# Performance work log

Hardware: AMD Instinct MI355X
Metric: run time of the kernel (lower is better)

The kernel has to match this reference:

```python
import jax, jax.numpy as jnp
import numpy as np

WH, WW = 7, 7           # window height/width
N = WH * WW             # tokens per window = 49
C = 768                 # num_channels
H = 24                  # num_heads
D = C // H              # head_dim = 32
B = 1024                # total windows (batch * windows-per-image)
NW = 64                 # windows per image (shift_mask leading dim)
EPS = 1e-5


def _relative_position_index():
    # Mirrors the torch buffer construction in __init__.
    coords = np.stack(np.meshgrid(np.arange(WH), np.arange(WW), indexing='ij'))  # [2,WH,WW]
    cf = coords.reshape(2, -1)                          # [2,N]
    rel = cf[:, :, None] - cf[:, None, :]               # [2,N,N]
    rel = rel.transpose(1, 2, 0).copy()                 # [N,N,2]
    rel[:, :, 0] += WH - 1
    rel[:, :, 1] += WW - 1
    rel[:, :, 0] *= 2 * WW - 1
    return jnp.asarray(rel.sum(-1), dtype=jnp.int32)    # [N,N]


def setup_inputs() -> dict:
    key = jax.random.key(0)
    ks = jax.random.split(key, 6)
    x = jax.random.normal(ks[0], (B, N, C), dtype=jnp.float32)
    shift_mask = jax.random.normal(ks[1], (NW, N, N), dtype=jnp.float32)
    w_qkv = jax.random.normal(ks[2], (3 * C, C), dtype=jnp.float32) * 0.02
    b_qkv = jnp.zeros((3 * C,), dtype=jnp.float32)
    w_proj = jax.random.normal(ks[3], (C, C), dtype=jnp.float32) * 0.02
    b_proj = jnp.zeros((C,), dtype=jnp.float32)
    rel_bias_table = jax.random.normal(ks[4], ((2 * WH - 1) * (2 * WW - 1), H), dtype=jnp.float32) * 0.02
    ln_g = jnp.ones((C,), dtype=jnp.float32)
    ln_b = jnp.zeros((C,), dtype=jnp.float32)
    rel_pos_index = _relative_position_index()
    return {
        'x': x, 'shift_mask': shift_mask,
        'w_qkv': w_qkv, 'b_qkv': b_qkv,
        'w_proj': w_proj, 'b_proj': b_proj,
        'rel_bias_table': rel_bias_table,
        'ln_g': ln_g, 'ln_b': ln_b,
        'rel_pos_index': rel_pos_index,
    }


def reference(x, shift_mask, w_qkv, b_qkv, w_proj, b_proj, rel_bias_table, ln_g, ln_b, rel_pos_index):
    B_, N_, C_ = x.shape
    # QKV projection: [B,N,3C] -> [3,B,H,N,D]
    qkv = (x @ w_qkv.T + b_qkv).reshape(B_, N_, 3, H, D).transpose(2, 0, 3, 1, 4)
    q, k, v = qkv[0], qkv[1], qkv[2]
    # Relative position bias gather: [N,N,H] -> [1,H,N,N]
    bias = rel_bias_table[rel_pos_index.reshape(-1)].reshape(N_, N_, H).transpose(2, 0, 1)[None]
    # Shift mask broadcast over batch repeats and heads: [B,1,N,N]
    mask = jnp.tile(shift_mask, (B_ // shift_mask.shape[0], 1, 1))[:, None]
    attn_bias = bias + mask  # [B,H,N,N]
    scale = 1.0 / np.sqrt(D).astype(np.float32)
    scores = jnp.einsum('bhnd,bhmd->bhnm', q, k) * scale + attn_bias
    attn = jax.nn.softmax(scores, axis=-1)
    out = jnp.einsum('bhnm,bhmd->bhnd', attn, v)       # [B,H,N,D]
    out = out.transpose(0, 2, 1, 3).reshape(B_, N_, C_)
    out = out @ w_proj.T + b_proj                      # dropout p=0 -> identity
    y = out + x
    mu = jnp.mean(y, axis=-1, keepdims=True)
    var = jnp.mean(jnp.square(y - mu), axis=-1, keepdims=True)
    return (y - mu) * jax.lax.rsqrt(var + EPS) * ln_g + ln_b
```

## Files before the change

kernel.cpp:

```cpp
#include <hip/hip_runtime.h>
#include <hip/hip_bf16.h>

#define SEQ 49
#define CH 768
#define NH 24
#define HD 32
#define NB 1024
#define NWIN 64
#define MTOT (NB*SEQ)

typedef __hip_bfloat16 bf16;
typedef __attribute__((ext_vector_type(8))) short short8;
typedef __attribute__((ext_vector_type(4))) short short4v;
typedef __attribute__((ext_vector_type(4))) float f32x4;

#define MD  ((size_t)MTOT * HD)
#define NHMD ((size_t)NH * MD)

__device__ __forceinline__ void gload16(const void* g, void* l) {
  __builtin_amdgcn_global_load_lds((__attribute__((address_space(1))) void*)g,
                                   (__attribute__((address_space(3))) void*)l,
                                   16, 0, 0);
}

__device__ __forceinline__ float bf2f(short s) {
  return __uint_as_float(((unsigned int)(unsigned short)s) << 16);
}

__global__ void cvt_bf16(const float* __restrict__ in, bf16* __restrict__ o, int n4) {
  int i = blockIdx.x * blockDim.x + threadIdx.x;
  if (i >= n4) return;
  float4 v = ((const float4*)in)[i];
  union { bf16 b[4]; short4 s; } u;
  u.b[0] = __float2bfloat16(v.x);
  u.b[1] = __float2bfloat16(v.y);
  u.b[2] = __float2bfloat16(v.z);
  u.b[3] = __float2bfloat16(v.w);
  ((short4*)o)[i] = u.s;
}

__global__ void build_comb(const float* __restrict__ table, const int* __restrict__ rpi,
                           const float* __restrict__ smask, float* __restrict__ comb) {
  int i = blockIdx.x * blockDim.x + threadIdx.x;
  int mn = i & 4095;
  int m = mn >> 6, n = mn & 63;
  int sh = i >> 12;
  int h = sh % NH;
  int s = sh / NH;
  float v = -1e30f;
  if (m < SEQ && n < SEQ)
    v = table[rpi[m * SEQ + n] * NH + h] + smask[s * SEQ * SEQ + m * SEQ + n];
  comb[i] = v;
}


__global__ __launch_bounds__(256) void qkv_gemm(
    const bf16* __restrict__ A, const bf16* __restrict__ Bw,
    const float* __restrict__ bias, bf16* __restrict__ C)
{
  __shared__ __align__(16) bf16 As[2 * 128 * 64];
  __shared__ __align__(16) bf16 Bs[2 * 128 * 64];
  const int tid = threadIdx.x;
  const int w = tid >> 6, l = tid & 63;
  const int lr = l & 15, lg = l >> 4;
  const int wm = w >> 1, wn = w & 1;

  const int flat = blockIdx.x;
  const int wg = (flat & 7) * 882 + (flat >> 3);
  const int bm = wg / 18, bn = wg - 18 * (wg / 18);

  const bf16* gA[4];
  const bf16* gB[4];
  int ldst[4];
#pragma unroll
  for (int j = 0; j < 4; j++) {
    int c = j * 256 + tid;
    int row = c >> 3, cpos = c & 7;
    int srcch = cpos ^ (row & 7);
    gA[j] = A + ((size_t)(bm * 128 + row)) * CH + srcch * 8;
    gB[j] = Bw + ((size_t)(bn * 128 + row)) * CH + srcch * 8;
    ldst[j] = c * 8;
  }

  f32x4 acc[4][4];
  f32x4 zero4 = {0.f, 0.f, 0.f, 0.f};
#pragma unroll
  for (int i = 0; i < 4; i++)
#pragma unroll
    for (int j = 0; j < 4; j++) acc[i][j] = zero4;

  int offA[4][2], offB[4][2];
#pragma unroll
  for (int mi = 0; mi < 4; mi++) {
#pragma unroll
    for (int ks = 0; ks < 2; ks++) {
      int rowa = 64 * wm + 16 * mi + lr;
      offA[mi][ks] = rowa * 64 + ((lg + 4 * ks) ^ (rowa & 7)) * 8;
      int rowb = 64 * wn + 16 * mi + lr;
      offB[mi][ks] = rowb * 64 + ((lg + 4 * ks) ^ (rowb & 7)) * 8;
    }
  }

#pragma unroll
  for (int j = 0; j < 4; j++) gload16(gA[j], As + ldst[j]);
#pragma unroll
  for (int j = 0; j < 4; j++) gload16(gB[j], Bs + ldst[j]);
#pragma unroll
  for (int j = 0; j < 4; j++) gload16(gA[j] + 64, As + 8192 + ldst[j]);
#pragma unroll
  for (int j = 0; j < 4; j++) gload16(gB[j] + 64, Bs + 8192 + ldst[j]);

  for (int t = 0; t < 12; ++t) {
    if (t < 11) asm volatile("s_waitcnt vmcnt(8)" ::: "memory");
    else        asm volatile("s_waitcnt vmcnt(0)" ::: "memory");
    __builtin_amdgcn_sched_barrier(0);
    __builtin_amdgcn_s_barrier();
    const int base = (t & 1) * 8192;
    const bf16* cA = As + base;
    const bf16* cB = Bs + base;
    short8 af[4][2], bfv[4][2];
#pragma unroll
    for (int mi = 0; mi < 4; mi++)
#pragma unroll
      for (int ks = 0; ks < 2; ks++) {
        af[mi][ks] = *(const short8*)(cA + offA[mi][ks]);
        bfv[mi][ks] = *(const short8*)(cB + offB[mi][ks]);
      }
    asm volatile("s_waitcnt lgkmcnt(0)" ::: "memory");
    __builtin_amdgcn_sched_barrier(0);
    __builtin_amdgcn_s_barrier();
    if (t < 10) {
      const int kk = (t + 2) * 64;
#pragma unroll
      for (int j = 0; j < 4; j++) gload16(gA[j] + kk, As + base + ldst[j]);
#pragma unroll
      for (int j = 0; j < 4; j++) gload16(gB[j] + kk, Bs + base + ldst[j]);
    }
    __builtin_amdgcn_s_setprio(1);
#pragma unroll
    for (int ks = 0; ks < 2; ks++)
#pragma unroll
      for (int mi = 0; mi < 4; mi++)
#pragma unroll
        for (int nj = 0; nj < 4; nj++)
          acc[mi][nj] = __builtin_amdgcn_mfma_f32_16x16x32_bf16(af[mi][ks], bfv[nj][ks], acc[mi][nj], 0, 0, 0);
    __builtin_amdgcn_s_setprio(0);
  }

  const float scale = 0.17677669529663687f;
  const int colbase = bn * 128 + 64 * wn;
  const int rowbase = bm * 128 + 64 * wm;
#pragma unroll
  for (int nj = 0; nj < 4; nj++) {
    const int cb16 = colbase + 16 * nj;
    const int sec = cb16 / 768;
    const int rem = cb16 - sec * 768;
    const int h = rem >> 5;
    const int dbase = rem & 31;
    float bv = bias[cb16 + lr];
    if (sec == 2) {
      const size_t vbase = 2 * NHMD + ((size_t)h * HD + dbase + lr) * MTOT;
#pragma unroll
      for (int mi = 0; mi < 4; mi++) {
        size_t row = rowbase + 16 * mi + 4 * lg;
        union { bf16 b[4]; short4 s; } u;
#pragma unroll
        for (int r = 0; r < 4; r++) u.b[r] = __float2bfloat16(acc[mi][nj][r] + bv);
        *(short4*)(C + vbase + row) = u.s;
      }
    } else {
      const float mul = (sec == 0) ? scale : 1.0f;
      const size_t base = (size_t)sec * NHMD + (size_t)h * MD + dbase + lr;
#pragma unroll
      for (int mi = 0; mi < 4; mi++) {
#pragma unroll
        for (int r = 0; r < 4; r++) {
          size_t row = rowbase + 16 * mi + 4 * lg + r;
          C[base + row * HD] = __float2bfloat16((acc[mi][nj][r] + bv) * mul);
        }
      }
    }
  }
}

__global__ __launch_bounds__(256) void attn_kernel(
    const bf16* __restrict__ qkvT, const float* __restrict__ comb,
    bf16* __restrict__ aout)
{
  __shared__ __align__(16) bf16 P[4][64 * 72];
  const int tid = threadIdx.x;
  const int w = tid >> 6, l = tid & 63;
  const int lr = l & 15, lg = l >> 4;
  const int b = blockIdx.x;
  const int h = blockIdx.y * 4 + w;
  const size_t rowb = (size_t)b * SEQ;
  f32x4 zero4 = {0.f, 0.f, 0.f, 0.f};

  const bf16* qb = qkvT + (size_t)h * MD + rowb * HD;
  const bf16* kb = qkvT + NHMD + (size_t)h * MD + rowb * HD;
  const bf16* vT = qkvT + 2 * NHMD + (size_t)h * HD * MTOT;

  short8 qf[4], kf[4];
#pragma unroll
  for (int mt = 0; mt < 4; mt++)
    qf[mt] = *(const short8*)(qb + (16 * mt + lr) * HD + 8 * lg);
#pragma unroll
  for (int nt = 0; nt < 4; nt++)
    kf[nt] = *(const short8*)(kb + (16 * nt + lr) * HD + 8 * lg);

  f32x4 s[4][4];
#pragma unroll
  for (int mt = 0; mt < 4; mt++)
#pragma unroll
    for (int nt = 0; nt < 4; nt++)
      s[mt][nt] = __builtin_amdgcn_mfma_f32_16x16x32_bf16(qf[mt], kf[nt], zero4, 0, 0, 0);

  short8 pb[2][2];
#pragma unroll
  for (int kt = 0; kt < 2; kt++)
#pragma unroll
    for (int dt = 0; dt < 2; dt++)
      pb[kt][dt] = *(const short8*)(vT + ((size_t)(16 * dt + lr)) * MTOT + rowb + 32 * kt + 8 * lg);

  const float* cb = comb + (((size_t)(b & (NWIN - 1)) * NH + h) << 12);
#pragma unroll
  for (int mt = 0; mt < 4; mt++)
#pragma unroll
    for (int nt = 0; nt < 4; nt++)
#pragma unroll
      for (int r = 0; r < 4; r++)
        s[mt][nt][r] += cb[((16 * mt + 4 * lg + r) << 6) + 16 * nt + lr];

  float mx[4][4];
#pragma unroll
  for (int mt = 0; mt < 4; mt++)
#pragma unroll
    for (int r = 0; r < 4; r++) {
      float m0 = fmaxf(fmaxf(s[mt][0][r], s[mt][1][r]), fmaxf(s[mt][2][r], s[mt][3][r]));
      m0 = fmaxf(m0, __shfl_xor(m0, 1, 64));
      m0 = fmaxf(m0, __shfl_xor(m0, 2, 64));
      m0 = fmaxf(m0, __shfl_xor(m0, 4, 64));
      m0 = fmaxf(m0, __shfl_xor(m0, 8, 64));
      mx[mt][r] = m0;
    }
  float inv[4][4];
#pragma unroll
  for (int mt = 0; mt < 4; mt++)
#pragma unroll
    for (int r = 0; r < 4; r++) {
      float t = 0.f;
#pragma unroll
      for (int nt = 0; nt < 4; nt++) {
        float e = __expf(s[mt][nt][r] - mx[mt][r]);
        s[mt][nt][r] = e;
        t += e;
      }
      t += __shfl_xor(t, 1, 64);
      t += __shfl_xor(t, 2, 64);
      t += __shfl_xor(t, 4, 64);
      t += __shfl_xor(t, 8, 64);
      inv[mt][r] = 1.0f / t;
    }

#pragma unroll
  for (int mt = 0; mt < 4; mt++)
#pragma unroll
    for (int nt = 0; nt < 4; nt++)
#pragma unroll
      for (int r = 0; r < 4; r++)
        P[w][(16 * mt + 4 * lg + r) * 72 + 16 * nt + lr] =
            __float2bfloat16(s[mt][nt][r]);

  f32x4 o[4][2];
#pragma unroll
  for (int mt = 0; mt < 4; mt++) { o[mt][0] = zero4; o[mt][1] = zero4; }
#pragma unroll
  for (int kt = 0; kt < 2; kt++) {
    short8 pa[4];
#pragma unroll
    for (int mt = 0; mt < 4; mt++)
      pa[mt] = *(const short8*)(&P[w][(16 * mt + lr) * 72 + 32 * kt + 8 * lg]);
#pragma unroll
    for (int mt = 0; mt < 4; mt++)
#pragma unroll
      for (int dt = 0; dt < 2; dt++)
        o[mt][dt] = __builtin_amdgcn_mfma_f32_16x16x32_bf16(pa[mt], pb[kt][dt], o[mt][dt], 0, 0, 0);
  }

#pragma unroll
  for (int mt = 0; mt < 4; mt++)
#pragma unroll
    for (int dt = 0; dt < 2; dt++)
#pragma unroll
      for (int r = 0; r < 4; r++) {
        int m = 16 * mt + 4 * lg + r;
        if (m < SEQ)
          aout[(rowb + m) * CH + h * HD + 16 * dt + lr] =
              __float2bfloat16(o[mt][dt][r] * inv[mt][r]);
      }
}

__global__ __launch_bounds__(256) void proj_gemm(
    const bf16* __restrict__ A, const bf16* __restrict__ Bw,
    const float* __restrict__ bias, const float* __restrict__ x,
    bf16* __restrict__ Y)
{
  __shared__ __align__(16) bf16 As[2 * 128 * 64];
  __shared__ __align__(16) bf16 Bs[2 * 128 * 64];
  const int tid = threadIdx.x;
  const int w = tid >> 6, l = tid & 63;
  const int lr = l & 15, lg = l >> 4;
  const int wm = w >> 1, wn = w & 1;

  const int flat = blockIdx.x;
  const int wg = (flat & 7) * 294 + (flat >> 3);
  const int bm = wg / 6, bn = wg - 6 * (wg / 6);

  const bf16* gA[4];
  const bf16* gB[4];
  int ldst[4];
#pragma unroll
  for (int j = 0; j < 4; j++) {
    int c = j * 256 + tid;
    int row = c >> 3, cpos = c & 7;
    int srcch = cpos ^ (row & 7);
    gA[j] = A + ((size_t)(bm * 128 + row)) * CH + srcch * 8;
    gB[j] = Bw + ((size_t)(bn * 128 + row)) * CH + srcch * 8;
    ldst[j] = c * 8;
  }

  f32x4 acc[4][4];
  f32x4 zero4 = {0.f, 0.f, 0.f, 0.f};
#pragma unroll
  for (int i = 0; i < 4; i++)
#pragma unroll
    for (int j = 0; j < 4; j++) acc[i][j] = zero4;

  int offA[4][2], offB[4][2];
#pragma unroll
  for (int mi = 0; mi < 4; mi++) {
#pragma unroll
    for (int ks = 0; ks < 2; ks++) {
      int rowa = 64 * wm + 16 * mi + lr;
      offA[mi][ks] = rowa * 64 + ((lg + 4 * ks) ^ (rowa & 7)) * 8;
      int rowb = 64 * wn + 16 * mi + lr;
      offB[mi][ks] = rowb * 64 + ((lg + 4 * ks) ^ (rowb & 7)) * 8;
    }
  }

#pragma unroll
  for (int j = 0; j < 4; j++) gload16(gA[j], As + ldst[j]);
#pragma unroll
  for (int j = 0; j < 4; j++) gload16(gB[j], Bs + ldst[j]);
#pragma unroll
  for (int j = 0; j < 4; j++) gload16(gA[j] + 64, As + 8192 + ldst[j]);
#pragma unroll
  for (int j = 0; j < 4; j++) gload16(gB[j] + 64, Bs + 8192 + ldst[j]);

  for (int t = 0; t < 12; ++t) {
    if (t < 11) asm volatile("s_waitcnt vmcnt(8)" ::: "memory");
    else        asm volatile("s_waitcnt vmcnt(0)" ::: "memory");
    __builtin_amdgcn_sched_barrier(0);
    __builtin_amdgcn_s_barrier();
    const int base = (t & 1) * 8192;
    const bf16* cA = As + base;
    const bf16* cB = Bs + base;
    short8 af[4][2], bfv[4][2];
#pragma unroll
    for (int mi = 0; mi < 4; mi++)
#pragma unroll
      for (int ks = 0; ks < 2; ks++) {
        af[mi][ks] = *(const short8*)(cA + offA[mi][ks]);
        bfv[mi][ks] = *(const short8*)(cB + offB[mi][ks]);
      }
    asm volatile("s_waitcnt lgkmcnt(0)" ::: "memory");
    __builtin_amdgcn_sched_barrier(0);
    __builtin_amdgcn_s_barrier();
    if (t < 10) {
      const int kk = (t + 2) * 64;
#pragma unroll
      for (int j = 0; j < 4; j++) gload16(gA[j] + kk, As + base + ldst[j]);
#pragma unroll
      for (int j = 0; j < 4; j++) gload16(gB[j] + kk, Bs + base + ldst[j]);
    }
    __builtin_amdgcn_s_setprio(1);
#pragma unroll
    for (int ks = 0; ks < 2; ks++)
#pragma unroll
      for (int mi = 0; mi < 4; mi++)
#pragma unroll
        for (int nj = 0; nj < 4; nj++)
          acc[mi][nj] = __builtin_amdgcn_mfma_f32_16x16x32_bf16(af[mi][ks], bfv[nj][ks], acc[mi][nj], 0, 0, 0);
    __builtin_amdgcn_s_setprio(0);
  }

  const int colbase = bn * 128 + 64 * wn;
  const int rowbase = bm * 128 + 64 * wm;
#pragma unroll
  for (int nj = 0; nj < 4; nj++) {
    int col = colbase + 16 * nj + lr;
    float bv = bias[col];
#pragma unroll
    for (int mi = 0; mi < 4; mi++) {
#pragma unroll
      for (int r = 0; r < 4; r++) {
        size_t row = rowbase + 16 * mi + 4 * lg + r;
        float v = acc[mi][nj][r] + bv + x[row * CH + col];
        Y[row * CH + col] = __float2bfloat16(v);
      }
    }
  }
}

__global__ __launch_bounds__(256) void ln_kernel(
    const bf16* __restrict__ Y, const float* __restrict__ g,
    const float* __restrict__ be, float* __restrict__ out)
{
  const int w = threadIdx.x >> 6, l = threadIdx.x & 63;
  const size_t r = (size_t)blockIdx.x * 4 + w;
  const bf16* yr = Y + r * CH;

  short8 a = *(const short8*)(yr + 8 * l);
  short4v b4 = *(const short4v*)(yr + 512 + 4 * l);
  float v[12];
#pragma unroll
  for (int j = 0; j < 8; j++) v[j] = bf2f(a[j]);
#pragma unroll
  for (int j = 0; j < 4; j++) v[8 + j] = bf2f(b4[j]);

  float s1 = 0.f, s2 = 0.f;
#pragma unroll
  for (int j = 0; j < 12; j++) { s1 += v[j]; s2 += v[j] * v[j]; }
#pragma unroll
  for (int m = 1; m <= 32; m <<= 1) {
    s1 += __shfl_xor(s1, m, 64);
    s2 += __shfl_xor(s2, m, 64);
  }
  float mu = s1 * (1.0f / 768.0f);
  float var = s2 * (1.0f / 768.0f) - mu * mu;
  float rs = rsqrtf(var + 1e-5f);

  float4 g0 = *(const float4*)(g + 8 * l);
  float4 g1 = *(const float4*)(g + 8 * l + 4);
  float4 g2 = *(const float4*)(g + 512 + 4 * l);
  float4 b0 = *(const float4*)(be + 8 * l);
  float4 b1 = *(const float4*)(be + 8 * l + 4);
  float4 b2 = *(const float4*)(be + 512 + 4 * l);

  float4 o0, o1, o2;
  o0.x = (v[0] - mu) * rs * g0.x + b0.x;
  o0.y = (v[1] - mu) * rs * g0.y + b0.y;
  o0.z = (v[2] - mu) * rs * g0.z + b0.z;
  o0.w = (v[3] - mu) * rs * g0.w + b0.w;
  o1.x = (v[4] - mu) * rs * g1.x + b1.x;
  o1.y = (v[5] - mu) * rs * g1.y + b1.y;
  o1.z = (v[6] - mu) * rs * g1.z + b1.z;
  o1.w = (v[7] - mu) * rs * g1.w + b1.w;
  o2.x = (v[8] - mu) * rs * g2.x + b2.x;
  o2.y = (v[9] - mu) * rs * g2.y + b2.y;
  o2.z = (v[10] - mu) * rs * g2.z + b2.z;
  o2.w = (v[11] - mu) * rs * g2.w + b2.w;

  float* orow = out + r * CH;
  *(float4*)(orow + 8 * l) = o0;
  *(float4*)(orow + 8 * l + 4) = o1;
  *(float4*)(orow + 512 + 4 * l) = o2;
}

extern "C" void kernel_launch(void* const* d_in, const int* in_sizes, int n_in,
                              void* d_out, int out_size, void* d_ws, size_t ws_size,
                              hipStream_t stream) {
  (void)in_sizes; (void)n_in; (void)out_size; (void)ws_size;
  const float* x     = (const float*)d_in[0];
  const float* smask = (const float*)d_in[1];
  const float* wqkv  = (const float*)d_in[2];
  const float* bqkv  = (const float*)d_in[3];
  const float* wproj = (const float*)d_in[4];
  const float* bproj = (const float*)d_in[5];
  const float* table = (const float*)d_in[6];
  const float* lng   = (const float*)d_in[7];
  const float* lnb   = (const float*)d_in[8];
  const int*   rpi   = (const int*)d_in[9];
  float* out = (float*)d_out;

  char* ws = (char*)d_ws;
  bf16*  xb   = (bf16*)(ws);
  bf16*  wqb  = (bf16*)(ws + 77070336);
  bf16*  wpb  = (bf16*)(ws + 80609280);
  float* comb = (float*)(ws + 81788928);
  bf16*  qkvT = (bf16*)(ws + 106954752);
  bf16*  aout = (bf16*)(ws);
  bf16*  yb   = (bf16*)(ws + 106954752);

  cvt_bf16<<<37632, 256, 0, stream>>>(x, xb, 9633792);
  cvt_bf16<<<1728, 256, 0, stream>>>(wqkv, wqb, 442368);
  cvt_bf16<<<576, 256, 0, stream>>>(wproj, wpb, 147456);
  build_comb<<<24576, 256, 0, stream>>>(table, rpi, smask, comb);
  qkv_gemm<<<7056, 256, 0, stream>>>(xb, wqb, bqkv, qkvT);
  attn_kernel<<<dim3(1024, 6), 256, 0, stream>>>(qkvT, comb, aout);
  proj_gemm<<<2352, 256, 0, stream>>>(aout, wpb, bproj, x, yb);
  ln_kernel<<<12544, 256, 0, stream>>>(yb, lng, lnb, out);
}
```

Baseline: 603.8 us.

## Enlarge QKV GEMM tile to 256x256 with 512 threads and 128KB LDS

The QKV GEMM moves from 128x128 tiles with 4 waves to 256x256 tiles with 8 waves, each computing 128x64. Shared memory becomes dynamic at 128KB for double-buffered A/B, and the XCD-aware block remap is updated for the new grid of 1764 blocks. The prefetch is restructured to issue the next K-slice at the top of each iteration, and fragments are loaded per k-step. The goal is higher arithmetic intensity and less global/LDS traffic per FLOP, at the cost of one block per CU, more accumulator registers and a shallower prefetch pipeline.

```diff
diff --git a/kernel.cpp b/kernel.cpp
--- a/kernel.cpp
+++ b/kernel.cpp
@@ -53,103 +53,105 @@
   comb[i] = v;
 }
 
-
-__global__ __launch_bounds__(256) void qkv_gemm(
+__global__ __launch_bounds__(512) void qkv_gemm(
     const bf16* __restrict__ A, const bf16* __restrict__ Bw,
     const float* __restrict__ bias, bf16* __restrict__ C)
 {
-  __shared__ __align__(16) bf16 As[2 * 128 * 64];
-  __shared__ __align__(16) bf16 Bs[2 * 128 * 64];
+  extern __shared__ __align__(16) bf16 lds[];
   const int tid = threadIdx.x;
   const int w = tid >> 6, l = tid & 63;
   const int lr = l & 15, lg = l >> 4;
-  const int wm = w >> 1, wn = w & 1;
+  const int wm = w >> 2, wn = w & 3;
 
   const int flat = blockIdx.x;
-  const int wg = (flat & 7) * 882 + (flat >> 3);
-  const int bm = wg / 18, bn = wg - 18 * (wg / 18);
+  const int xcd = flat & 7, lid = flat >> 3;
+  const int wgid = (xcd < 4 ? xcd * 221 : 884 + (xcd - 4) * 220) + lid;
+  const int bm = wgid / 9, bn = wgid - 9 * bm;
 
   const bf16* gA[4];
   const bf16* gB[4];
   int ldst[4];
 #pragma unroll
   for (int j = 0; j < 4; j++) {
-    int c = j * 256 + tid;
+    int c = j * 512 + tid;
     int row = c >> 3, cpos = c & 7;
     int srcch = cpos ^ (row & 7);
-    gA[j] = A + ((size_t)(bm * 128 + row)) * CH + srcch * 8;
-    gB[j] = Bw + ((size_t)(bn * 128 + row)) * CH + srcch * 8;
+    gA[j] = A + ((size_t)(bm * 256 + row)) * CH + srcch * 8;
+    gB[j] = Bw + ((size_t)(bn * 256 + row)) * CH + srcch * 8;
     ldst[j] = c * 8;
   }
 
-  f32x4 acc[4][4];
+  f32x4 acc[8][4];
   f32x4 zero4 = {0.f, 0.f, 0.f, 0.f};
 #pragma unroll
-  for (int i = 0; i < 4; i++)
+  for (int i = 0; i < 8; i++)
 #pragma unroll
     for (int j = 0; j < 4; j++) acc[i][j] = zero4;
 
-  int offA[4][2], offB[4][2];
-#pragma unroll
-  for (int mi = 0; mi < 4; mi++) {
+  int offA[8][2], offB[4][2];
+#pragma unroll
+  for (int mi = 0; mi < 8; mi++)
 #pragma unroll
     for (int ks = 0; ks < 2; ks++) {
-      int rowa = 64 * wm + 16 * mi + lr;
+      int rowa = wm * 128 + mi * 16 + lr;
       offA[mi][ks] = rowa * 64 + ((lg + 4 * ks) ^ (rowa & 7)) * 8;
-      int rowb = 64 * wn + 16 * mi + lr;
-      offB[mi][ks] = rowb * 64 + ((lg + 4 * ks) ^ (rowb & 7)) * 8;
-    }
-  }
-
-#pragma unroll
-  for (int j = 0; j < 4; j++) gload16(gA[j], As + ldst[j]);
-#pragma unroll
-  for (int j = 0; j < 4; j++) gload16(gB[j], Bs + ldst[j]);
-#pragma unroll
-  for (int j = 0; j < 4; j++) gload16(gA[j] + 64, As + 8192 + ldst[j]);
-#pragma unroll
-  for (int j = 0; j < 4; j++) gload16(gB[j] + 64, Bs + 8192 + ldst[j]);
+    }
+#pragma unroll
+  for (int nj = 0; nj < 4; nj++)
+#pragma unroll
+    for (int ks = 0; ks < 2; ks++) {
+      int rowb = wn * 64 + nj * 16 + lr;
+      offB[nj][ks] = rowb * 64 + ((lg + 4 * ks) ^ (rowb & 7)) * 8;
+    }
+
+#pragma unroll
+  for (int j = 0; j < 4; j++) gload16(gA[j], lds + ldst[j]);
+#pragma unroll
+  for (int j = 0; j < 4; j++) gload16(gB[j], lds + 32768 + ldst[j]);
 
   for (int t = 0; t < 12; ++t) {
-    if (t < 11) asm volatile("s_waitcnt vmcnt(8)" ::: "memory");
-    else        asm volatile("s_waitcnt vmcnt(0)" ::: "memory");
+    const int cur = t & 1;
+    if (t < 11) {
+      const int kk = (t + 1) * 64;
+      bf16* nA = lds + (cur ^ 1) * 16384;
+      bf16* nB = lds + 32768 + (cur ^ 1) * 16384;
+#pragma unroll
+      for (int j = 0; j < 4; j++) gload16(gA[j] + kk, nA + ldst[j]);
+#pragma unroll
+      for (int j = 0; j < 4; j++) gload16(gB[j] + kk, nB + ldst[j]);
+      asm volatile("s_waitcnt vmcnt(8)" ::: "memory");
+    } else {
+      asm volatile("s_waitcnt vmcnt(0)" ::: "memory");
+    }
     __builtin_amdgcn_sched_barrier(0);
     __builtin_amdgcn_s_barrier();
-    const int base = (t & 1) * 8192;
-    const bf16* cA = As + base;
-    const bf16* cB = Bs + base;
-    short8 af[4][2], bfv[4][2];
-#pragma unroll
-    for (int mi = 0; mi < 4; mi++)
-#pragma unroll
-      for (int ks = 0; ks < 2; ks++) {
-        af[mi][ks] = *(const short8*)(cA + offA[mi][ks]);
-        bfv[mi][ks] = *(const short8*)(cB + offB[mi][ks]);
-      }
+    __builtin_amdgcn_sched_barrier(0);
+    const bf16* cA = lds + cur * 16384;
+    const bf16* cB = lds + 32768 + cur * 16384;
+#pragma unroll
+    for (int ks = 0; ks < 2; ks++) {
+      short8 af[8], bfv[4];
+#pragma unroll
+      for (int mi = 0; mi < 8; mi++) af[mi] = *(const short8*)(cA + offA[mi][ks]);
+#pragma unroll
+      for (int nj = 0; nj < 4; nj++) bfv[nj] = *(const short8*)(cB + offB[nj][ks]);
+      __builtin_amdgcn_s_setprio(1);
+#pragma unroll
+      for (int mi = 0; mi < 8; mi++)
+#pragma unroll
+        for (int nj = 0; nj < 4; nj++)
+          acc[mi][nj] = __builtin_amdgcn_mfma_f32_16x16x32_bf16(af[mi], bfv[nj], acc[mi][nj], 0, 0, 0);
+      __builtin_amdgcn_s_setprio(0);
+    }
     asm volatile("s_waitcnt lgkmcnt(0)" ::: "memory");
     __builtin_amdgcn_sched_barrier(0);
     __builtin_amdgcn_s_barrier();
-    if (t < 10) {
-      const int kk = (t + 2) * 64;
-#pragma unroll
-      for (int j = 0; j < 4; j++) gload16(gA[j] + kk, As + base + ldst[j]);
-#pragma unroll
-      for (int j = 0; j < 4; j++) gload16(gB[j] + kk, Bs + base + ldst[j]);
-    }
-    __builtin_amdgcn_s_setprio(1);
-#pragma unroll
-    for (int ks = 0; ks < 2; ks++)
-#pragma unroll
-      for (int mi = 0; mi < 4; mi++)
-#pragma unroll
-        for (int nj = 0; nj < 4; nj++)
-          acc[mi][nj] = __builtin_amdgcn_mfma_f32_16x16x32_bf16(af[mi][ks], bfv[nj][ks], acc[mi][nj], 0, 0, 0);
-    __builtin_amdgcn_s_setprio(0);
+    __builtin_amdgcn_sched_barrier(0);
   }
 
   const float scale = 0.17677669529663687f;
-  const int colbase = bn * 128 + 64 * wn;
-  const int rowbase = bm * 128 + 64 * wm;
+  const int colbase = bn * 256 + 64 * wn;
+  const int rowbase = bm * 256 + 128 * wm;
 #pragma unroll
   for (int nj = 0; nj < 4; nj++) {
     const int cb16 = colbase + 16 * nj;
@@ -161,7 +163,7 @@
     if (sec == 2) {
       const size_t vbase = 2 * NHMD + ((size_t)h * HD + dbase + lr) * MTOT;
 #pragma unroll
-      for (int mi = 0; mi < 4; mi++) {
+      for (int mi = 0; mi < 8; mi++) {
         size_t row = rowbase + 16 * mi + 4 * lg;
         union { bf16 b[4]; short4 s; } u;
 #pragma unroll
@@ -172,7 +174,7 @@
       const float mul = (sec == 0) ? scale : 1.0f;
       const size_t base = (size_t)sec * NHMD + (size_t)h * MD + dbase + lr;
 #pragma unroll
-      for (int mi = 0; mi < 4; mi++) {
+      for (int mi = 0; mi < 8; mi++) {
 #pragma unroll
         for (int r = 0; r < 4; r++) {
           size_t row = rowbase + 16 * mi + 4 * lg + r;
@@ -496,7 +498,7 @@
   cvt_bf16<<<1728, 256, 0, stream>>>(wqkv, wqb, 442368);
   cvt_bf16<<<576, 256, 0, stream>>>(wproj, wpb, 147456);
   build_comb<<<24576, 256, 0, stream>>>(table, rpi, smask, comb);
-  qkv_gemm<<<7056, 256, 0, stream>>>(xb, wqb, bqkv, qkvT);
+  qkv_gemm<<<1764, 512, 131072, stream>>>(xb, wqb, bqkv, qkvT);
   attn_kernel<<<dim3(1024, 6), 256, 0, stream>>>(qkvT, comb, aout);
   proj_gemm<<<2352, 256, 0, stream>>>(aout, wpb, bproj, x, yb);
   ln_kernel<<<12544, 256, 0, stream>>>(yb, lng, lnb, out);
```

Result: faster. 577.0 us (-4.4%).
